# Kernel optimization log

Measured on AMD Instinct MI355X. Metric: run time of the kernel, lower is better.

Reference implementation:

```python
import jax, jax.numpy as jnp
import numpy as np

NUM_LAYERS = 4      # GraphCNN num_layers -> 3 GraphConvolution layers
NUM_CLUSTERS = 512  # == hidden_dim
MAX_ITERS = 10


def mish(x):
    return x * jnp.tanh(jax.nn.softplus(x))


def _sqdist(X, C):
    # squared euclidean distances [N, K]; argmin identical to torch.cdist argmin
    x2 = jnp.sum(X * X, axis=1, keepdims=True)          # [N, 1]
    c2 = jnp.sum(C * C, axis=1)[None, :]                # [1, K]
    return x2 + c2 - 2.0 * (X @ C.T)


def ctod(X):
    """k-means (init = first K rows, MAX_ITERS iters) -> one-hot assignments [N, K]."""
    N = X.shape[0]
    centers0 = X[:NUM_CLUSTERS]
    labels0 = jnp.zeros((N,), dtype=jnp.int32)

    def body(carry, _):
        centers, _ = carry
        labels = jnp.argmin(_sqdist(X, centers), axis=1)       # [N]
        oh = jax.nn.one_hot(labels, NUM_CLUSTERS, dtype=X.dtype)  # [N, K]
        counts = oh.sum(axis=0)                                # [K]
        sums = oh.T @ X                                        # [K, D]
        means = sums / jnp.maximum(counts, 1.0)[:, None]
        # keep old center for empty clusters (torch: only update if cluster non-empty)
        new_centers = jnp.where(counts[:, None] > 0, means, centers)
        return (new_centers, labels), None

    (_, labels), _ = jax.lax.scan(body, (centers0, labels0), None, length=MAX_ITERS)
    labels = jax.lax.stop_gradient(labels)  # argmin/one-hot is non-differentiable
    return jax.nn.one_hot(labels, NUM_CLUSTERS, dtype=X.dtype)


def _graph_forward(X, adj, W, b):
    h = X
    for _ in range(NUM_LAYERS - 1):
        h = ctod(h)                 # [N, K] one-hot
        h = mish(adj @ h)           # GraphConvolution with mish
    h = mish(adj @ (h @ W) + b)     # lastGCN (GCN layer, use_bias=True)
    return h                        # [N, hidden]


def setup_inputs() -> dict:
    key = jax.random.key(0)
    ks = jax.random.split(key, 4)
    B, N, D, H, O = 8, 4096, 512, 512, 10
    x = jax.random.normal(ks[0], (B, N, D), dtype=jnp.float32)
    # adj_lap: normalized-laplacian-like operator; scale to keep activations sane
    adj = jax.random.normal(ks[1], (B, N, N), dtype=jnp.float32) / np.sqrt(N)
    W = jax.random.normal(ks[2], (H, H), dtype=jnp.float32) * (1.0 / np.sqrt(H))
    b = jnp.zeros((H,), dtype=jnp.float32)
    Wp = jax.random.normal(ks[3], (H, O), dtype=jnp.float32) * (1.0 / np.sqrt(H))
    bp = jnp.zeros((O,), dtype=jnp.float32)
    return {"x": x, "adj": adj, "W": W, "b": b, "Wp": Wp, "bp": bp}


def reference(x, adj, W, b, Wp, bp):
    # per-graph GCN stack (vmapped over the batch of graphs)
    h = jax.vmap(_graph_forward, in_axes=(0, 0, None, None))(x, adj, W, b)  # [B, N, H]
    # graph_pool with 'sum' pooling (elem=1): sum node embeddings per graph
    pooled = h.sum(axis=1)                                                  # [B, H]
    # final linear prediction (dropout is identity in eval mode)
    return pooled @ Wp + bp                                                 # [B, O]
```

## Files before the change

kernel.cpp:

```cpp
#include <hip/hip_runtime.h>
#include <math.h>

#define BB 8
#define NN 4096
#define DD 512
#define KK 512
#define MAXIT 10

__device__ __forceinline__ float mish_f(float x) {
  float sp = (x > 20.f) ? x : log1pf(expf(x));
  return x * tanhf(sp);
}

__global__ void transpose512(const float* __restrict__ W, float* __restrict__ Wt) {
  __shared__ float tile[32][33];
  int bx = blockIdx.x, by = blockIdx.y;
  int tx = threadIdx.x, ty = threadIdx.y;
  tile[ty][tx] = W[(by*32+ty)*512 + bx*32+tx];
  __syncthreads();
  Wt[(bx*32+ty)*512 + by*32+tx] = tile[tx][ty];
}

__global__ void init_centers(const float* __restrict__ X, float* __restrict__ centers,
                             float* __restrict__ c2) {
  int k = blockIdx.x, b = blockIdx.y, l = threadIdx.x;
  const float4* src = (const float4*)(X + ((size_t)b*NN + k)*DD) + l*2;
  float4* dst = (float4*)(centers + ((size_t)b*KK + k)*DD) + l*2;
  float4 a0 = src[0], a1 = src[1];
  dst[0] = a0; dst[1] = a1;
  float s = a0.x*a0.x + a0.y*a0.y + a0.z*a0.z + a0.w*a0.w
          + a1.x*a1.x + a1.y*a1.y + a1.z*a1.z + a1.w*a1.w;
  #pragma unroll
  for (int m = 32; m >= 1; m >>= 1) s += __shfl_xor(s, m);
  if (l == 0) c2[b*KK + k] = s;
}

template<int EPI>
__global__ __launch_bounds__(256)
void gemm_bt(const float* __restrict__ A, const float* __restrict__ Bmat,
             int Kd, long long sA, long long sB,
             const float* __restrict__ c2, int* __restrict__ labels,
             float* __restrict__ Gt,
             const float* __restrict__ bias, float* __restrict__ pooled)
{
  __shared__ float Xs[64*68];
  __shared__ float Cs[128*68];
  const int t = threadIdx.x;
  const int tx = t & 31, ty = t >> 5;
  const int b = blockIdx.y;
  const int r0 = blockIdx.x * 64;
  const float* Ab = A + (size_t)b * sA;
  const float* Bb = Bmat + (size_t)b * sB;

  float bestd[8]; int bestk[8];
  if (EPI == 0) {
    #pragma unroll
    for (int r = 0; r < 8; ++r) { bestd[r] = 3.4e38f; bestk[r] = 0; }
  }

  for (int c0 = 0; c0 < 512; c0 += 128) {
    float acc[8][4];
    #pragma unroll
    for (int r = 0; r < 8; ++r)
      #pragma unroll
      for (int c = 0; c < 4; ++c) acc[r][c] = 0.f;

    for (int k0 = 0; k0 < Kd; k0 += 64) {
      __syncthreads();
      #pragma unroll
      for (int s = 0; s < 4; ++s) {
        int f = t + s*256;
        int row = f >> 4, k4 = f & 15;
        float4 v = *(const float4*)&Ab[(size_t)(r0+row)*Kd + k0 + 4*k4];
        *(float4*)&Xs[row*68 + 4*k4] = v;
      }
      #pragma unroll
      for (int s = 0; s < 8; ++s) {
        int f = t + s*256;
        int cl = f >> 4, k4 = f & 15;
        float4 v = *(const float4*)&Bb[(size_t)(c0+cl)*Kd + k0 + 4*k4];
        *(float4*)&Cs[cl*68 + 4*k4] = v;
      }
      __syncthreads();
      #pragma unroll 4
      for (int kk = 0; kk < 64; kk += 4) {
        float4 xv[8], cv[4];
        #pragma unroll
        for (int r = 0; r < 8; ++r) xv[r] = *(const float4*)&Xs[(ty+8*r)*68 + kk];
        #pragma unroll
        for (int c = 0; c < 4; ++c) cv[c] = *(const float4*)&Cs[(tx+32*c)*68 + kk];
        #pragma unroll
        for (int r = 0; r < 8; ++r)
          #pragma unroll
          for (int c = 0; c < 4; ++c) {
            acc[r][c] = fmaf(xv[r].x, cv[c].x, acc[r][c]);
            acc[r][c] = fmaf(xv[r].y, cv[c].y, acc[r][c]);
            acc[r][c] = fmaf(xv[r].z, cv[c].z, acc[r][c]);
            acc[r][c] = fmaf(xv[r].w, cv[c].w, acc[r][c]);
          }
      }
    }

    if (EPI == 0) {
      float c2v[4];
      #pragma unroll
      for (int c = 0; c < 4; ++c) c2v[c] = c2[b*512 + c0 + tx + 32*c];
      #pragma unroll
      for (int r = 0; r < 8; ++r)
        #pragma unroll
        for (int c = 0; c < 4; ++c) {
          float d = fmaf(-2.f, acc[r][c], c2v[c]);
          int col = c0 + tx + 32*c;
          if (d < bestd[r]) { bestd[r] = d; bestk[r] = col; }
        }
    } else if (EPI == 1) {
      __syncthreads();
      #pragma unroll
      for (int r = 0; r < 8; ++r)
        #pragma unroll
        for (int c = 0; c < 4; ++c)
          Cs[(tx+32*c)*65 + ty + 8*r] = acc[r][c];
      __syncthreads();
      #pragma unroll
      for (int s = 0; s < 8; ++s) {
        int f = t + s*256;
        int cl = f >> 4, r4 = f & 15;
        float4 v;
        v.x = Cs[cl*65 + 4*r4+0]; v.y = Cs[cl*65 + 4*r4+1];
        v.z = Cs[cl*65 + 4*r4+2]; v.w = Cs[cl*65 + 4*r4+3];
        *(float4*)&Gt[((size_t)b*512 + c0+cl)*4096 + r0 + 4*r4] = v;
      }
    } else {
      float rs[4];
      #pragma unroll
      for (int c = 0; c < 4; ++c) {
        float bv = bias[c0 + tx + 32*c];
        float s = 0.f;
        #pragma unroll
        for (int r = 0; r < 8; ++r) s += mish_f(acc[r][c] + bv);
        rs[c] = s;
      }
      __syncthreads();
      #pragma unroll
      for (int c = 0; c < 4; ++c) Cs[ty*128 + tx + 32*c] = rs[c];
      __syncthreads();
      if (t < 128) {
        float s = 0.f;
        #pragma unroll
        for (int g = 0; g < 8; ++g) s += Cs[g*128 + t];
        atomicAdd(&pooled[b*512 + c0 + t], s);
      }
      __syncthreads();
    }
  }

  if (EPI == 0) {
    #pragma unroll
    for (int r = 0; r < 8; ++r) {
      float d = bestd[r]; int k = bestk[r];
      #pragma unroll
      for (int m = 16; m >= 1; m >>= 1) {
        float d2 = __shfl_xor(d, m); int k2 = __shfl_xor(k, m);
        if (d2 < d || (d2 == d && k2 < k)) { d = d2; k = k2; }
      }
      if (tx == 0) labels[b*NN + r0 + ty + 8*r] = k;
    }
  }
}

__global__ void build_members(const int* __restrict__ labels, int* __restrict__ counts,
                              int* __restrict__ offsets, int* __restrict__ members) {
  __shared__ int cnt[KK];
  __shared__ int scan[KK];
  __shared__ int cur[KK];
  int b = blockIdx.x, t = threadIdx.x;
  if (t < KK) cnt[t] = 0;
  __syncthreads();
  for (int i = t; i < NN; i += 1024) atomicAdd(&cnt[labels[b*NN + i]], 1);
  __syncthreads();
  if (t < KK) scan[t] = cnt[t];
  __syncthreads();
  for (int s = 1; s < KK; s <<= 1) {
    int v = 0;
    if (t < KK && t >= s) v = scan[t - s];
    __syncthreads();
    if (t < KK && t >= s) scan[t] += v;
    __syncthreads();
  }
  if (t < KK) {
    int off = scan[t] - cnt[t];
    counts[b*KK + t] = cnt[t];
    offsets[b*KK + t] = off;
    cur[t] = off;
  }
  __syncthreads();
  for (int i = t; i < NN; i += 1024) {
    int lab = labels[b*NN + i];
    int p = atomicAdd(&cur[lab], 1);
    members[b*NN + p] = i;
  }
}

__global__ void update_centers(const float* __restrict__ X, const int* __restrict__ counts,
                               const int* __restrict__ offsets, const int* __restrict__ members,
                               float* __restrict__ centers, float* __restrict__ c2) {
  int k = blockIdx.x, b = blockIdx.y, l = threadIdx.x;
  int cnt = counts[b*KK + k];
  if (cnt == 0) return;
  int off = offsets[b*KK + k];
  const float* Xb = X + (size_t)b*NN*DD;
  float4 a0 = {0,0,0,0}, a1 = {0,0,0,0};
  for (int m = 0; m < cnt; ++m) {
    int i = members[b*NN + off + m];
    const float4* r = (const float4*)(Xb + (size_t)i*DD) + l*2;
    float4 v0 = r[0], v1 = r[1];
    a0.x+=v0.x; a0.y+=v0.y; a0.z+=v0.z; a0.w+=v0.w;
    a1.x+=v1.x; a1.y+=v1.y; a1.z+=v1.z; a1.w+=v1.w;
  }
  float fc = (float)cnt;
  a0.x/=fc; a0.y/=fc; a0.z/=fc; a0.w/=fc;
  a1.x/=fc; a1.y/=fc; a1.z/=fc; a1.w/=fc;
  float4* dst = (float4*)(centers + ((size_t)b*KK + k)*DD) + l*2;
  dst[0] = a0; dst[1] = a1;
  float s = a0.x*a0.x+a0.y*a0.y+a0.z*a0.z+a0.w*a0.w
          + a1.x*a1.x+a1.y*a1.y+a1.z*a1.z+a1.w*a1.w;
  #pragma unroll
  for (int m = 32; m >= 1; m >>= 1) s += __shfl_xor(s, m);
  if (l == 0) c2[b*KK + k] = s;
}

__global__ void gather_mish(const float* __restrict__ adj, const int* __restrict__ counts,
                            const int* __restrict__ offsets, const int* __restrict__ members,
                            float* __restrict__ hout) {
  __shared__ float row[NN];
  int i = blockIdx.x, b = blockIdx.y, t = threadIdx.x;
  const float4* ar = (const float4*)(adj + ((size_t)b*NN + i)*NN);
  #pragma unroll
  for (int s = 0; s < 4; ++s) {
    int f = t + s*256;
    *(float4*)&row[4*f] = ar[f];
  }
  __syncthreads();
  #pragma unroll
  for (int h = 0; h < 2; ++h) {
    int k = t + h*256;
    int cnt = counts[b*KK + k];
    int off = offsets[b*KK + k];
    float s = 0.f;
    for (int m = 0; m < cnt; ++m) s += row[members[b*NN + off + m]];
    hout[((size_t)b*NN + i)*DD + k] = mish_f(s);
  }
}

__global__ void final_out(const float* __restrict__ pooled, const float* __restrict__ Wp,
                          const float* __restrict__ bp, float* __restrict__ out) {
  int b = blockIdx.x, l = threadIdx.x;
  float acc[10];
  #pragma unroll
  for (int o = 0; o < 10; ++o) acc[o] = 0.f;
  for (int k = l; k < 512; k += 64) {
    float p = pooled[b*512 + k];
    #pragma unroll
    for (int o = 0; o < 10; ++o) acc[o] = fmaf(p, Wp[k*10+o], acc[o]);
  }
  #pragma unroll
  for (int o = 0; o < 10; ++o) {
    float s = acc[o];
    #pragma unroll
    for (int m = 32; m >= 1; m >>= 1) s += __shfl_xor(s, m);
    if (l == 0) out[b*10+o] = s + bp[o];
  }
}

extern "C" void kernel_launch(void* const* d_in, const int* in_sizes, int n_in,
                              void* d_out, int out_size, void* d_ws, size_t ws_size,
                              hipStream_t stream) {
  const float* x    = (const float*)d_in[0];
  const float* adj  = (const float*)d_in[1];
  const float* W    = (const float*)d_in[2];
  const float* bias = (const float*)d_in[3];
  const float* Wp   = (const float*)d_in[4];
  const float* bp   = (const float*)d_in[5];
  float* out = (float*)d_out;

  char* ws = (char*)d_ws;
  size_t off = 0;
  auto alloc = [&](size_t bytes) {
    void* p = ws + off;
    off += (bytes + 255) & ~(size_t)255;
    return p;
  };
  float* hbuf    = (float*)alloc((size_t)BB*NN*DD*4);
  float* Gt      = (float*)alloc((size_t)BB*DD*NN*4);
  float* centers = (float*)alloc((size_t)BB*KK*DD*4);
  float* c2      = (float*)alloc((size_t)BB*KK*4);
  int*   labels  = (int*)alloc((size_t)BB*NN*4);
  int*   counts  = (int*)alloc((size_t)BB*KK*4);
  int*   offsets = (int*)alloc((size_t)BB*KK*4);
  int*   members = (int*)alloc((size_t)BB*NN*4);
  float* pooled  = (float*)alloc((size_t)BB*DD*4);
  float* Wt      = (float*)alloc((size_t)DD*DD*4);

  transpose512<<<dim3(16,16), dim3(32,32), 0, stream>>>(W, Wt);

  const float* Xcur = x;
  for (int layer = 0; layer < 3; ++layer) {
    init_centers<<<dim3(KK,BB), dim3(64), 0, stream>>>(Xcur, centers, c2);
    for (int it = 0; it < MAXIT; ++it) {
      gemm_bt<0><<<dim3(64,BB), dim3(256), 0, stream>>>(
          Xcur, centers, DD, (long long)NN*DD, (long long)KK*DD,
          c2, labels, nullptr, nullptr, nullptr);
      build_members<<<dim3(BB), dim3(1024), 0, stream>>>(labels, counts, offsets, members);
      if (it < MAXIT-1)
        update_centers<<<dim3(KK,BB), dim3(64), 0, stream>>>(
            Xcur, counts, offsets, members, centers, c2);
    }
    gather_mish<<<dim3(NN,BB), dim3(256), 0, stream>>>(adj, counts, offsets, members, hbuf);
    Xcur = hbuf;
  }

  gemm_bt<1><<<dim3(64,BB), dim3(256), 0, stream>>>(
      Xcur, Wt, DD, (long long)NN*DD, 0LL,
      nullptr, nullptr, Gt, nullptr, nullptr);

  hipMemsetAsync(pooled, 0, (size_t)BB*DD*4, stream);

  gemm_bt<2><<<dim3(64,BB), dim3(256), 0, stream>>>(
      adj, Gt, NN, (long long)NN*NN, (long long)DD*NN,
      nullptr, nullptr, nullptr, bias, pooled);

  final_out<<<dim3(BB), dim3(64), 0, stream>>>(pooled, Wp, bp, out);
}
```

Before: 14.94 ms.

## Retile GEMM to 256x128 blocks with column-split grid and atomic argmin

The shared GEMM kernel now uses 256x128 output tiles with 16x8 per-thread accumulators and a K-step of 32. It splits the 512 columns across a grid dimension instead of looping over them inside one block, which gives more register reuse per shared-memory load and more independent blocks. Because a block no longer sees every center, the k-means argmin is merged across column blocks with a 64-bit atomicMin on packed (ordered distance, index) keys. build_members resets those keys after reading them. The cost is heavy register pressure (128 accumulators under launch_bounds 256,2) and extra atomic traffic.

```diff
diff --git a/kernel.cpp b/kernel.cpp
--- a/kernel.cpp
+++ b/kernel.cpp
@@ -10,6 +10,11 @@
 __device__ __forceinline__ float mish_f(float x) {
   float sp = (x > 20.f) ? x : log1pf(expf(x));
   return x * tanhf(sp);
+}
+
+__device__ __forceinline__ unsigned int fkey(float f) {
+  unsigned int u = __float_as_uint(f);
+  return (u & 0x80000000u) ? ~u : (u | 0x80000000u);
 }
 
 __global__ void transpose512(const float* __restrict__ W, float* __restrict__ Wt) {
@@ -36,139 +41,138 @@
 }
 
 template<int EPI>
-__global__ __launch_bounds__(256)
+__global__ __launch_bounds__(256, 2)
 void gemm_bt(const float* __restrict__ A, const float* __restrict__ Bmat,
              int Kd, long long sA, long long sB,
-             const float* __restrict__ c2, int* __restrict__ labels,
+             const float* __restrict__ c2, unsigned long long* __restrict__ packed,
              float* __restrict__ Gt,
              const float* __restrict__ bias, float* __restrict__ pooled)
 {
-  __shared__ float Xs[64*68];
-  __shared__ float Cs[128*68];
+  __shared__ float smem[13824];
+  float* As = smem;
+  float* Bs = smem + 9216;
   const int t = threadIdx.x;
-  const int tx = t & 31, ty = t >> 5;
-  const int b = blockIdx.y;
-  const int r0 = blockIdx.x * 64;
+  const int tx = t & 15, ty = t >> 4;
+  const int b = blockIdx.z;
+  const int r0 = blockIdx.x * 256;
+  const int c0 = blockIdx.y * 128;
   const float* Ab = A + (size_t)b * sA;
   const float* Bb = Bmat + (size_t)b * sB;
 
-  float bestd[8]; int bestk[8];
+  float acc[16][8];
+  #pragma unroll
+  for (int r = 0; r < 16; ++r)
+    #pragma unroll
+    for (int c = 0; c < 8; ++c) acc[r][c] = 0.f;
+
+  for (int k0 = 0; k0 < Kd; k0 += 32) {
+    __syncthreads();
+    #pragma unroll
+    for (int s = 0; s < 8; ++s) {
+      int f = t + s*256;
+      int row = f >> 3, k4 = (f & 7) << 2;
+      *(float4*)&As[row*36 + k4] = *(const float4*)&Ab[(size_t)(r0+row)*Kd + k0 + k4];
+    }
+    #pragma unroll
+    for (int s = 0; s < 4; ++s) {
+      int f = t + s*256;
+      int row = f >> 3, k4 = (f & 7) << 2;
+      *(float4*)&Bs[row*36 + k4] = *(const float4*)&Bb[(size_t)(c0+row)*Kd + k0 + k4];
+    }
+    __syncthreads();
+    for (int kk = 0; kk < 32; kk += 4) {
+      float4 cv[8];
+      #pragma unroll
+      for (int c = 0; c < 8; ++c) cv[c] = *(const float4*)&Bs[(tx+16*c)*36 + kk];
+      #pragma unroll
+      for (int rg = 0; rg < 4; ++rg) {
+        float4 xv[4];
+        #pragma unroll
+        for (int q = 0; q < 4; ++q)
+          xv[q] = *(const float4*)&As[(ty + 16*(4*rg+q))*36 + kk];
+        #pragma unroll
+        for (int q = 0; q < 4; ++q) {
+          #pragma unroll
+          for (int c = 0; c < 8; ++c) {
+            float a = acc[4*rg+q][c];
+            a = fmaf(xv[q].x, cv[c].x, a);
+            a = fmaf(xv[q].y, cv[c].y, a);
+            a = fmaf(xv[q].z, cv[c].z, a);
+            a = fmaf(xv[q].w, cv[c].w, a);
+            acc[4*rg+q][c] = a;
+          }
+        }
+      }
+    }
+  }
+
   if (EPI == 0) {
-    #pragma unroll
-    for (int r = 0; r < 8; ++r) { bestd[r] = 3.4e38f; bestk[r] = 0; }
-  }
-
-  for (int c0 = 0; c0 < 512; c0 += 128) {
-    float acc[8][4];
-    #pragma unroll
-    for (int r = 0; r < 8; ++r)
-      #pragma unroll
-      for (int c = 0; c < 4; ++c) acc[r][c] = 0.f;
-
-    for (int k0 = 0; k0 < Kd; k0 += 64) {
+    float c2v[8];
+    #pragma unroll
+    for (int c = 0; c < 8; ++c) c2v[c] = c2[b*KK + c0 + tx + 16*c];
+    #pragma unroll
+    for (int r = 0; r < 16; ++r) {
+      float bd = 3.4e38f; int bk = 0;
+      #pragma unroll
+      for (int c = 0; c < 8; ++c) {
+        float d = fmaf(-2.f, acc[r][c], c2v[c]);
+        int col = c0 + tx + 16*c;
+        if (d < bd) { bd = d; bk = col; }
+      }
+      #pragma unroll
+      for (int m = 1; m <= 8; m <<= 1) {
+        float d2 = __shfl_xor(bd, m); int k2 = __shfl_xor(bk, m);
+        if (d2 < bd || (d2 == bd && k2 < bk)) { bd = d2; bk = k2; }
+      }
+      if (tx == 0) {
+        unsigned long long key = ((unsigned long long)fkey(bd) << 32) | (unsigned int)bk;
+        atomicMin(&packed[(size_t)b*NN + r0 + ty + 16*r], key);
+      }
+    }
+  } else if (EPI == 1) {
+    #pragma unroll
+    for (int rh = 0; rh < 4; ++rh) {
       __syncthreads();
       #pragma unroll
-      for (int s = 0; s < 4; ++s) {
-        int f = t + s*256;
-        int row = f >> 4, k4 = f & 15;
-        float4 v = *(const float4*)&Ab[(size_t)(r0+row)*Kd + k0 + 4*k4];
-        *(float4*)&Xs[row*68 + 4*k4] = v;
-      }
+      for (int q = 0; q < 4; ++q)
+        #pragma unroll
+        for (int c = 0; c < 8; ++c)
+          smem[(tx+16*c)*68 + ty + 16*q] = acc[4*rh+q][c];
+      __syncthreads();
       #pragma unroll
       for (int s = 0; s < 8; ++s) {
         int f = t + s*256;
-        int cl = f >> 4, k4 = f & 15;
-        float4 v = *(const float4*)&Bb[(size_t)(c0+cl)*Kd + k0 + 4*k4];
-        *(float4*)&Cs[cl*68 + 4*k4] = v;
-      }
-      __syncthreads();
-      #pragma unroll 4
-      for (int kk = 0; kk < 64; kk += 4) {
-        float4 xv[8], cv[4];
-        #pragma unroll
-        for (int r = 0; r < 8; ++r) xv[r] = *(const float4*)&Xs[(ty+8*r)*68 + kk];
-        #pragma unroll
-        for (int c = 0; c < 4; ++c) cv[c] = *(const float4*)&Cs[(tx+32*c)*68 + kk];
-        #pragma unroll
-        for (int r = 0; r < 8; ++r)
-          #pragma unroll
-          for (int c = 0; c < 4; ++c) {
-            acc[r][c] = fmaf(xv[r].x, cv[c].x, acc[r][c]);
-            acc[r][c] = fmaf(xv[r].y, cv[c].y, acc[r][c]);
-            acc[r][c] = fmaf(xv[r].z, cv[c].z, acc[r][c]);
-            acc[r][c] = fmaf(xv[r].w, cv[c].w, acc[r][c]);
-          }
-      }
-    }
-
-    if (EPI == 0) {
-      float c2v[4];
-      #pragma unroll
-      for (int c = 0; c < 4; ++c) c2v[c] = c2[b*512 + c0 + tx + 32*c];
-      #pragma unroll
-      for (int r = 0; r < 8; ++r)
-        #pragma unroll
-        for (int c = 0; c < 4; ++c) {
-          float d = fmaf(-2.f, acc[r][c], c2v[c]);
-          int col = c0 + tx + 32*c;
-          if (d < bestd[r]) { bestd[r] = d; bestk[r] = col; }
-        }
-    } else if (EPI == 1) {
-      __syncthreads();
-      #pragma unroll
-      for (int r = 0; r < 8; ++r)
-        #pragma unroll
-        for (int c = 0; c < 4; ++c)
-          Cs[(tx+32*c)*65 + ty + 8*r] = acc[r][c];
-      __syncthreads();
-      #pragma unroll
-      for (int s = 0; s < 8; ++s) {
-        int f = t + s*256;
-        int cl = f >> 4, r4 = f & 15;
+        int col = f >> 4, r4 = (f & 15) << 2;
         float4 v;
-        v.x = Cs[cl*65 + 4*r4+0]; v.y = Cs[cl*65 + 4*r4+1];
-        v.z = Cs[cl*65 + 4*r4+2]; v.w = Cs[cl*65 + 4*r4+3];
-        *(float4*)&Gt[((size_t)b*512 + c0+cl)*4096 + r0 + 4*r4] = v;
-      }
-    } else {
-      float rs[4];
-      #pragma unroll
-      for (int c = 0; c < 4; ++c) {
-        float bv = bias[c0 + tx + 32*c];
-        float s = 0.f;
-        #pragma unroll
-        for (int r = 0; r < 8; ++r) s += mish_f(acc[r][c] + bv);
-        rs[c] = s;
-      }
-      __syncthreads();
-      #pragma unroll
-      for (int c = 0; c < 4; ++c) Cs[ty*128 + tx + 32*c] = rs[c];
-      __syncthreads();
-      if (t < 128) {
-        float s = 0.f;
-        #pragma unroll
-        for (int g = 0; g < 8; ++g) s += Cs[g*128 + t];
-        atomicAdd(&pooled[b*512 + c0 + t], s);
-      }
-      __syncthreads();
-    }
-  }
-
-  if (EPI == 0) {
-    #pragma unroll
-    for (int r = 0; r < 8; ++r) {
-      float d = bestd[r]; int k = bestk[r];
-      #pragma unroll
-      for (int m = 16; m >= 1; m >>= 1) {
-        float d2 = __shfl_xor(d, m); int k2 = __shfl_xor(k, m);
-        if (d2 < d || (d2 == d && k2 < k)) { d = d2; k = k2; }
-      }
-      if (tx == 0) labels[b*NN + r0 + ty + 8*r] = k;
-    }
-  }
-}
-
-__global__ void build_members(const int* __restrict__ labels, int* __restrict__ counts,
+        v.x = smem[col*68 + r4+0]; v.y = smem[col*68 + r4+1];
+        v.z = smem[col*68 + r4+2]; v.w = smem[col*68 + r4+3];
+        *(float4*)&Gt[((size_t)b*KK + c0+col)*NN + r0 + rh*64 + r4] = v;
+      }
+    }
+  } else {
+    float rs[8];
+    #pragma unroll
+    for (int c = 0; c < 8; ++c) {
+      float bv = bias[c0 + tx + 16*c];
+      float s = 0.f;
+      #pragma unroll
+      for (int r = 0; r < 16; ++r) s += mish_f(acc[r][c] + bv);
+      rs[c] = s;
+    }
+    __syncthreads();
+    #pragma unroll
+    for (int c = 0; c < 8; ++c) smem[ty*128 + tx + 16*c] = rs[c];
+    __syncthreads();
+    if (t < 128) {
+      float s = 0.f;
+      #pragma unroll
+      for (int g = 0; g < 16; ++g) s += smem[g*128 + t];
+      atomicAdd(&pooled[b*KK + c0 + t], s);
+    }
+  }
+}
+
+__global__ void build_members(unsigned long long* __restrict__ packed, int* __restrict__ counts,
                               int* __restrict__ offsets, int* __restrict__ members) {
   __shared__ int cnt[KK];
   __shared__ int scan[KK];
@@ -176,7 +180,8 @@
   int b = blockIdx.x, t = threadIdx.x;
   if (t < KK) cnt[t] = 0;
   __syncthreads();
-  for (int i = t; i < NN; i += 1024) atomicAdd(&cnt[labels[b*NN + i]], 1);
+  for (int i = t; i < NN; i += 1024)
+    atomicAdd(&cnt[(int)(packed[(size_t)b*NN + i] & 0xffffffffull)], 1);
   __syncthreads();
   if (t < KK) scan[t] = cnt[t];
   __syncthreads();
@@ -195,9 +200,10 @@
   }
   __syncthreads();
   for (int i = t; i < NN; i += 1024) {
-    int lab = labels[b*NN + i];
+    int lab = (int)(packed[(size_t)b*NN + i] & 0xffffffffull);
     int p = atomicAdd(&cur[lab], 1);
     members[b*NN + p] = i;
+    packed[(size_t)b*NN + i] = ~0ull;
   }
 }
 
@@ -294,7 +300,7 @@
   float* Gt      = (float*)alloc((size_t)BB*DD*NN*4);
   float* centers = (float*)alloc((size_t)BB*KK*DD*4);
   float* c2      = (float*)alloc((size_t)BB*KK*4);
-  int*   labels  = (int*)alloc((size_t)BB*NN*4);
+  unsigned long long* packed = (unsigned long long*)alloc((size_t)BB*NN*8);
   int*   counts  = (int*)alloc((size_t)BB*KK*4);
   int*   offsets = (int*)alloc((size_t)BB*KK*4);
   int*   members = (int*)alloc((size_t)BB*NN*4);
@@ -302,15 +308,16 @@
   float* Wt      = (float*)alloc((size_t)DD*DD*4);
 
   transpose512<<<dim3(16,16), dim3(32,32), 0, stream>>>(W, Wt);
+  hipMemsetAsync(packed, 0xFF, (size_t)BB*NN*8, stream);
 
   const float* Xcur = x;
   for (int layer = 0; layer < 3; ++layer) {
     init_centers<<<dim3(KK,BB), dim3(64), 0, stream>>>(Xcur, centers, c2);
     for (int it = 0; it < MAXIT; ++it) {
-      gemm_bt<0><<<dim3(64,BB), dim3(256), 0, stream>>>(
+      gemm_bt<0><<<dim3(16,4,BB), dim3(256), 0, stream>>>(
           Xcur, centers, DD, (long long)NN*DD, (long long)KK*DD,
-          c2, labels, nullptr, nullptr, nullptr);
-      build_members<<<dim3(BB), dim3(1024), 0, stream>>>(labels, counts, offsets, members);
+          c2, packed, nullptr, nullptr, nullptr);
+      build_members<<<dim3(BB), dim3(1024), 0, stream>>>(packed, counts, offsets, members);
       if (it < MAXIT-1)
         update_centers<<<dim3(KK,BB), dim3(64), 0, stream>>>(
             Xcur, counts, offsets, members, centers, c2);
@@ -319,13 +326,13 @@
     Xcur = hbuf;
   }
 
-  gemm_bt<1><<<dim3(64,BB), dim3(256), 0, stream>>>(
+  gemm_bt<1><<<dim3(16,4,BB), dim3(256), 0, stream>>>(
       Xcur, Wt, DD, (long long)NN*DD, 0LL,
       nullptr, nullptr, Gt, nullptr, nullptr);
 
   hipMemsetAsync(pooled, 0, (size_t)BB*DD*4, stream);
 
-  gemm_bt<2><<<dim3(64,BB), dim3(256), 0, stream>>>(
+  gemm_bt<2><<<dim3(16,4,BB), dim3(256), 0, stream>>>(
       adj, Gt, NN, (long long)NN*NN, (long long)DD*NN,
       nullptr, nullptr, nullptr, bias, pooled);
 
```

Result: faster. 12.26 ms (-17.9%).
